# Optimization experiments

Hardware: AMD Instinct MI355X
Metric: run time of the kernel (lower is better)

The kernel has to match this reference:

```python
import jax, jax.numpy as jnp
import numpy as np

E, C_IN, NUM_CLASSES = 4, 3, 100
HW = 32
C1, C2, GC = 64, 128, 16
FC_IN = C2 * (HW // 4) * (HW // 4)  # 128*8*8 = 8192


def _conv(x, w, b):
    # x: [B,Cin,H,W], w: [Cout,Cin,3,3] -> [B,Cout,H,W] (SAME padding)
    y = jax.lax.conv_general_dilated(x, w, (1, 1), 'SAME',
                                     dimension_numbers=('NCHW', 'OIHW', 'NCHW'))
    return y + b[None, :, None, None]


def _maxpool2(x):
    return jax.lax.reduce_window(x, -jnp.inf, jax.lax.max,
                                 (1, 1, 2, 2), (1, 1, 2, 2), 'VALID')


def setup_inputs() -> dict:
    key = jax.random.key(0)
    ks = jax.random.split(key, 12)
    s = lambda k, shape, fan: (jax.random.normal(k, shape, jnp.float32) / np.sqrt(fan))
    return {
        'x': jax.random.normal(ks[0], (1024, C_IN, HW, HW), jnp.float32),
        # gating network
        'gate_cw': s(ks[1], (GC, C_IN, 3, 3), C_IN * 9),
        'gate_cb': jnp.zeros((GC,), jnp.float32),
        'gate_fw': s(ks[2], (E, GC), GC),
        'gate_fb': jnp.zeros((E,), jnp.float32),
        # stacked expert params [E, ...]
        'e_c1w': s(ks[3], (E, C1, C_IN, 3, 3), C_IN * 9),
        'e_c1b': jnp.zeros((E, C1), jnp.float32),
        'e_c2w': s(ks[4], (E, C2, C1, 3, 3), C1 * 9),
        'e_c2b': jnp.zeros((E, C2), jnp.float32),
        'e_fw': s(ks[5], (E, NUM_CLASSES, FC_IN), FC_IN),
        'e_fb': jnp.zeros((E, NUM_CLASSES), jnp.float32),
    }


def reference(x, gate_cw, gate_cb, gate_fw, gate_fb,
              e_c1w, e_c1b, e_c2w, e_c2b, e_fw, e_fb):
    B = x.shape[0]
    # --- gating: conv -> relu -> global avg pool -> linear -> softmax ---
    g = jax.nn.relu(_conv(x, gate_cw, gate_cb))            # [B,GC,H,W]
    g = g.mean(axis=(2, 3))                                # [B,GC]
    router_probs = jax.nn.softmax(g @ gate_fw.T + gate_fb) # [B,E]

    best_weights = router_probs.max(axis=1)                # [B]
    best_indices = jnp.argmax(router_probs, axis=1)        # [B]

    # --- hard top-1 dispatch: mask-and-combine (same math as gather/scatter) ---
    final_output = jnp.zeros((B, NUM_CLASSES), x.dtype)
    for e in range(E):  # fixed small expert count, structurally distinct params
        h = jax.nn.relu(_conv(x, e_c1w[e], e_c1b[e]))      # [B,64,32,32]
        h = _maxpool2(h)                                   # [B,64,16,16]
        h = jax.nn.relu(_conv(h, e_c2w[e], e_c2b[e]))      # [B,128,16,16]
        h = _maxpool2(h)                                   # [B,128,8,8]
        logits = h.reshape(B, -1) @ e_fw[e].T + e_fb[e]    # [B,100]
        mask = (best_indices == e)[:, None]
        final_output = final_output + jnp.where(
            mask, logits * best_weights[:, None], 0.0)

    mean_probs = router_probs.mean(axis=0)
    aux_loss = jnp.mean((mean_probs - 1.0 / E) ** 2)
    return final_output, router_probs, aux_loss
```

## Files before the change

kernel.cpp:

```cpp
#include <hip/hip_runtime.h>
#include <hip/hip_bf16.h>
#include <cstdint>


#define B_TOT 1024

typedef __attribute__((ext_vector_type(8))) short short8;
typedef __attribute__((ext_vector_type(16))) float f32x16;

__device__ __forceinline__ ushort f2bf(float f) {
  uint32_t u = __float_as_uint(f);
  u += 0x7fffu + ((u >> 16) & 1u);
  return (ushort)(u >> 16);
}

__global__ __launch_bounds__(256) void k_wprep(const float* __restrict__ w2,
                                               ushort* __restrict__ wp) {
  const int i = blockIdx.x * 256 + threadIdx.x;
  const int j = i & 7;
  const int cout = (i >> 3) & 127;
  const int kb = (i >> 10) & 7;
  const int kkE = i >> 13;
  const int kk = kkE - (kkE / 9) * 9;
  const int e = kkE / 9;
  const int ci = kb * 8 + j;
  const float f = w2[(size_t)(((e * 128 + cout) * 64 + ci) * 9) + kk];
  wp[i] = f2bf(f);
}

__global__ __launch_bounds__(256) void k_w1prep(const float* __restrict__ w1,
                                                ushort* __restrict__ wA) {
  const int i = blockIdx.x * 256 + threadIdx.x;
  const int j = i & 7;
  const int cout = (i >> 3) & 63;
  const int kb = (i >> 9) & 3;
  const int e = i >> 11;
  const int k = kb * 8 + j;
  float f = 0.f;
  if (k < 27) {
    const int ci = k / 9;
    const int kk = k - ci * 9;
    f = w1[(size_t)(((e * 64 + cout) * 3 + ci) * 9) + kk];
  }
  wA[i] = f2bf(f);
}

__global__ __launch_bounds__(256) void k_wfc(const float* __restrict__ efw,
                                             ushort* __restrict__ wfc) {
  const int i = blockIdx.x * 256 + threadIdx.x;
  const int j = i & 7;
  const int cout = (i >> 3) & 127;
  const int kb = (i >> 10) & 1023;
  const int e = i >> 20;
  const int k = kb * 8 + j;
  float f = 0.f;
  if (cout < 100) f = efw[((size_t)(e * 100 + cout)) * 8192 + k];
  wfc[i] = f2bf(f);
}

__global__ __launch_bounds__(256, 2) void k_gate(
    const float* __restrict__ x, const float* __restrict__ gcw,
    const float* __restrict__ gcb, float* __restrict__ g_mean) {
  __shared__ float xs[3 * 34 * 34];
  __shared__ float red[4 * 16];
  const int b = blockIdx.x;
  const int t = threadIdx.x;
  const float* xb = x + (size_t)b * 3072;

  for (int c = t; c < 3468; c += 256) {
    const int ci = c / 1156;
    const int rem = c - ci * 1156;
    const int y = rem / 34;
    const int xx = rem - y * 34;
    const int gy = y - 1, gx = xx - 1;
    float v = 0.f;
    if (gy >= 0 && gy < 32 && gx >= 0 && gx < 32) v = xb[ci * 1024 + gy * 32 + gx];
    xs[c] = v;
  }
  __syncthreads();

  const int r = t >> 3;
  const int c0 = (t & 7) * 4;

  float accp[16][4];
#pragma unroll
  for (int c = 0; c < 16; c++)
#pragma unroll
    for (int p = 0; p < 4; p++) accp[c][p] = 0.f;

#pragma unroll
  for (int ci = 0; ci < 3; ci++) {
    float pv[3][6];
#pragma unroll
    for (int dy = 0; dy < 3; dy++) {
      const float* row = xs + ci * 1156 + (r + dy) * 34 + c0;
#pragma unroll
      for (int dx = 0; dx < 6; dx++) pv[dy][dx] = row[dx];
    }
#pragma unroll
    for (int c = 0; c < 16; c++) {
      const float* wr = gcw + (c * 3 + ci) * 9;
#pragma unroll
      for (int ky = 0; ky < 3; ky++)
#pragma unroll
        for (int kx = 0; kx < 3; kx++) {
          const float wv = wr[ky * 3 + kx];
#pragma unroll
          for (int p = 0; p < 4; p++)
            accp[c][p] += wv * pv[ky][kx + p];
        }
    }
  }

  float sums[16];
#pragma unroll
  for (int c = 0; c < 16; c++) {
    const float bb = gcb[c];
    float s = 0.f;
#pragma unroll
    for (int p = 0; p < 4; p++) s += fmaxf(accp[c][p] + bb, 0.f);
    sums[c] = s;
  }

  const int wave = t >> 6, lane = t & 63;
#pragma unroll
  for (int c = 0; c < 16; c++) {
    float v = sums[c];
    for (int o = 32; o > 0; o >>= 1) v += __shfl_down(v, o);
    if (lane == 0) red[wave * 16 + c] = v;
  }
  __syncthreads();
  if (t < 16) {
    g_mean[b * 16 + t] =
        (red[t] + red[16 + t] + red[32 + t] + red[48 + t]) * (1.f / 1024.f);
  }
}

__global__ __launch_bounds__(256) void k_route(
    const float* __restrict__ g_mean, const float* __restrict__ gfw,
    const float* __restrict__ gfb, float* __restrict__ probs,
    float* __restrict__ best_w, int* __restrict__ best_idx,
    int* __restrict__ off_g, int* __restrict__ counts_g,
    int* __restrict__ order, float* __restrict__ aux_out) {
  __shared__ int cnt[4], ofs[5], cl[4];
  __shared__ short bidx[1024];
  __shared__ float red[16];
  const int t = threadIdx.x;
  if (t < 4) { cnt[t] = 0; cl[t] = 0; }
  __syncthreads();

  float asum[4] = {0.f, 0.f, 0.f, 0.f};
  for (int s = t; s < B_TOT; s += 256) {
    float g[16];
#pragma unroll
    for (int c = 0; c < 16; c++) g[c] = g_mean[s * 16 + c];
    float lg[4];
#pragma unroll
    for (int e = 0; e < 4; e++) {
      float sum = gfb[e];
#pragma unroll
      for (int c = 0; c < 16; c++) sum += g[c] * gfw[e * 16 + c];
      lg[e] = sum;
    }
    const float m = fmaxf(fmaxf(lg[0], lg[1]), fmaxf(lg[2], lg[3]));
    float ex[4], ssum = 0.f;
#pragma unroll
    for (int e = 0; e < 4; e++) { ex[e] = expf(lg[e] - m); ssum += ex[e]; }
    const float inv = 1.f / ssum;
    float p[4];
#pragma unroll
    for (int e = 0; e < 4; e++) {
      p[e] = ex[e] * inv;
      probs[s * 4 + e] = p[e];
      asum[e] += p[e];
    }
    int bi = 0; float bp = p[0];
#pragma unroll
    for (int e = 1; e < 4; e++) if (p[e] > bp) { bp = p[e]; bi = e; }
    best_w[s] = bp;
    best_idx[s] = bi;
    bidx[s] = (short)bi;
    atomicAdd(&cnt[bi], 1);
  }
  __syncthreads();

  if (t == 0) {
    int o = 0;
#pragma unroll
    for (int e = 0; e < 4; e++) { ofs[e] = o; o += ((cnt[e] + 31) & ~31); }
    ofs[4] = o;
#pragma unroll
    for (int i = 0; i < 5; i++) off_g[i] = ofs[i];
#pragma unroll
    for (int e = 0; e < 4; e++) counts_g[e] = cnt[e];
  }
  __syncthreads();

  for (int s = t; s < B_TOT; s += 256) {
    const int e2 = bidx[s];
    const int slot = ofs[e2] + atomicAdd(&cl[e2], 1);
    order[slot] = s;
  }

  const int wave = t >> 6, lane = t & 63;
#pragma unroll
  for (int e = 0; e < 4; e++) {
    float v = asum[e];
    for (int o = 32; o > 0; o >>= 1) v += __shfl_down(v, o);
    if (lane == 0) red[wave * 4 + e] = v;
  }
  __syncthreads();
  if (t == 0) {
    float aux = 0.f;
#pragma unroll
    for (int e = 0; e < 4; e++) {
      const float mp = (red[e] + red[4 + e] + red[8 + e] + red[12 + e]) * (1.f / 1024.f);
      const float d = mp - 0.25f;
      aux += d * d;
    }
    aux_out[0] = aux * 0.25f;
  }
}

__global__ __launch_bounds__(256) void k_conv1(
    const float* __restrict__ x, const ushort* __restrict__ wA,
    const float* __restrict__ b1, const int* __restrict__ best_idx,
    ushort* __restrict__ h1q) {
  __shared__ ushort xs[1020];
  __shared__ __align__(16) ushort Bl[256 * 32];
  const int blk = blockIdx.x;
  const int b = blk >> 2;
  const int q = blk & 3;
  const int t = threadIdx.x;
  const int e = __builtin_amdgcn_readfirstlane(best_idx[b]);
  const float* xb = x + (size_t)b * 3072;
  const float* b1e = b1 + (size_t)e * 64;

  for (int c = t; c < 1020; c += 256) {
    const int ci = c / 340;
    const int rem = c - ci * 340;
    const int hr = rem / 34;
    const int hc = rem - hr * 34;
    const int gr = 8 * q + hr - 1, gc = hc - 1;
    float v = 0.f;
    if (gr >= 0 && gr < 32 && gc >= 0 && gc < 32) v = xb[ci * 1024 + gr * 32 + gc];
    xs[c] = f2bf(v);
  }
  __syncthreads();

  {
    const int rr = t >> 5, cc = t & 31;
    ushort us[32];
#pragma unroll
    for (int k = 0; k < 32; k++) {
      ushort v = 0;
      if (k < 27) {
        const int ci = k / 9;
        const int tap = k - ci * 9;
        const int dy = tap / 3, dx = tap - dy * 3;
        v = xs[ci * 340 + (rr + dy) * 34 + cc + dx];
      }
      us[k] = v;
    }
    uint4 pk[2];
    uint* pu = (uint*)pk;
#pragma unroll
    for (int w = 0; w < 8; w++)
      pu[w] = (uint)us[w * 2] | ((uint)us[w * 2 + 1] << 16);
    *(uint4*)(Bl + t * 32) = pk[0];
    *(uint4*)(Bl + t * 32 + 8) = pk[1];
    uint4 pk2[2];
    uint* pu2 = (uint*)pk2;
#pragma unroll
    for (int w = 0; w < 8; w++)
      pu2[w] = (uint)us[16 + w * 2] | ((uint)us[16 + w * 2 + 1] << 16);
    *(uint4*)(Bl + t * 32 + 16) = pk2[0];
    *(uint4*)(Bl + t * 32 + 24) = pk2[1];
  }
  __syncthreads();

  const int lane = t & 63;
  const int wv = t >> 6;
  const int g = wv & 1;
  const int nh = wv >> 1;
  const int ln = lane & 31;
  const int half = lane >> 5;

  const short8 af0 = *(const short8*)(wA + (size_t)(((e * 4 + half) * 64) + g * 32 + ln) * 8);
  const short8 af1 = *(const short8*)(wA + (size_t)(((e * 4 + 2 + half) * 64) + g * 32 + ln) * 8);

  f32x16 acc[4];
#pragma unroll
  for (int tt = 0; tt < 4; tt++)
#pragma unroll
    for (int i = 0; i < 16; i++) acc[tt][i] = 0.f;

#pragma unroll
  for (int tt = 0; tt < 4; tt++) {
    const ushort* bcol = Bl + (size_t)((nh * 4 + tt) * 32 + ln) * 32;
    const short8 b0 = *(const short8*)(bcol + half * 8);
    const short8 b1v = *(const short8*)(bcol + 16 + half * 8);
    acc[tt] = __builtin_amdgcn_mfma_f32_32x32x16_bf16(af0, b0, acc[tt], 0, 0, 0);
    acc[tt] = __builtin_amdgcn_mfma_f32_32x32x16_bf16(af1, b1v, acc[tt], 0, 0, 0);
  }

  float bias[16];
#pragma unroll
  for (int r = 0; r < 16; r++)
    bias[r] = b1e[g * 32 + (r & 3) + 8 * (r >> 2) + 4 * half];

  const int pc = ln >> 1;
#pragma unroll
  for (int j = 0; j < 2; j++) {
    float pw[16];
#pragma unroll
    for (int r = 0; r < 16; r++) {
      float v = fmaxf(acc[2 * j][r], acc[2 * j + 1][r]);
      v = fmaxf(v, __shfl_xor(v, 1));
      pw[r] = fmaxf(v + bias[r], 0.f);
    }
    if ((lane & 1) == 0) {
      const int pos = (4 * q + nh * 2 + j) * 16 + pc;
      ushort* dst = h1q + (size_t)b * 16384 + pos * 8 + 4 * half;
#pragma unroll
      for (int rg = 0; rg < 4; rg++) {
        uint2 pk;
        pk.x = (uint)f2bf(pw[rg * 4 + 0]) | ((uint)f2bf(pw[rg * 4 + 1]) << 16);
        pk.y = (uint)f2bf(pw[rg * 4 + 2]) | ((uint)f2bf(pw[rg * 4 + 3]) << 16);
        *(uint2*)(dst + (g * 4 + rg) * 2048) = pk;
      }
    }
  }
}

__global__ __launch_bounds__(256, 2) void k_conv2(
    const ushort* __restrict__ h1q, const ushort* __restrict__ wp,
    const float* __restrict__ b2, const int* __restrict__ best_idx,
    ushort* __restrict__ h2q) {
  __shared__ uint4 st[1440];
  const int blk = blockIdx.x;
  const int b = blk >> 1;
  const int q = blk & 1;
  const int t = threadIdx.x;
  const int e = __builtin_amdgcn_readfirstlane(best_idx[b]);
  const ushort* wpe = wp + (size_t)e * 73728;

  for (int c = t; c < 1440; c += 256) {
    const int row = c / 144;
    const int rem = c - row * 144;
    const int cig = rem / 18;
    const int col = rem - cig * 18;
    const int gy = 8 * q - 1 + row, gx = col - 1;
    uint4 v = make_uint4(0u, 0u, 0u, 0u);
    if (gy >= 0 && gy < 16 && gx >= 0 && gx < 16)
      v = *(const uint4*)(h1q + (size_t)b * 16384 + cig * 2048 + (gy * 16 + gx) * 8);
    st[c] = v;
  }
  __syncthreads();

  const int lane = t & 63;
  const int wv = t >> 6;
  const int g = wv & 1;
  const int h = wv >> 1;
  const int half = lane >> 5;
  const int n = lane & 31;
  const int drow = n >> 4;
  const int col15 = n & 15;
  const int cm0 = g * 64;

  f32x16 acc[2][2];
#pragma unroll
  for (int m = 0; m < 2; m++)
#pragma unroll
    for (int nt = 0; nt < 2; nt++)
#pragma unroll
      for (int i = 0; i < 16; i++) acc[m][nt][i] = 0.f;

  const short* sbs = (const short*)st;
  const ushort* abase = wpe + (size_t)(half * 128 + cm0 + n) * 8;

  short8 a0[4], a1[4];
#pragma unroll
  for (int c4 = 0; c4 < 4; c4++) {
    a0[c4] = *(const short8*)(abase + c4 * 2048);
    a1[c4] = *(const short8*)(abase + c4 * 2048 + 256);
  }

#pragma unroll
  for (int kk = 0; kk < 9; kk++) {
    const int ky = kk / 3;
    const int kx = kk - ky * 3;
#pragma unroll
    for (int c4 = 0; c4 < 4; c4++) {
      const int kb = c4 * 2 + half;
#pragma unroll
      for (int nt = 0; nt < 2; nt++) {
        const int rin = 4 * h + 2 * nt + drow + ky;
        const int cin = col15 + kx;
        const short8 bf = *(const short8*)(sbs + ((rin * 8 + kb) * 18 + cin) * 8);
        acc[0][nt] = __builtin_amdgcn_mfma_f32_32x32x16_bf16(a0[c4], bf, acc[0][nt], 0, 0, 0);
        acc[1][nt] = __builtin_amdgcn_mfma_f32_32x32x16_bf16(a1[c4], bf, acc[1][nt], 0, 0, 0);
      }
      if (kk < 8) {
        a0[c4] = *(const short8*)(abase + (kk + 1) * 8192 + c4 * 2048);
        a1[c4] = *(const short8*)(abase + (kk + 1) * 8192 + c4 * 2048 + 256);
      }
    }
  }
  __syncthreads();

  ushort* pls = (ushort*)st;
#pragma unroll
  for (int m = 0; m < 2; m++)
#pragma unroll
    for (int nt = 0; nt < 2; nt++) {
#pragma unroll
      for (int r = 0; r < 16; r++) {
        float v = acc[m][nt][r];
        v = fmaxf(v, __shfl_xor(v, 1));
        v = fmaxf(v, __shfl_xor(v, 16));
        if ((lane & 17) == 0) {
          const int rowm = (r & 3) + 8 * (r >> 2) + 4 * half;
          const int cout = cm0 + m * 32 + rowm;
          const int prl = 2 * h + nt;
          const int pc = (n >> 1) & 7;
          pls[cout * 32 + prl * 8 + pc] = f2bf(fmaxf(v + b2[e * 128 + cout], 0.f));
        }
      }
    }
  __syncthreads();

  {
#pragma unroll
    for (int p = 0; p < 2; p++) {
      const int f16 = p * 256 + t;
      const int flat = f16 * 8;
      const int cout = flat >> 5;
      const int pos32 = flat & 31;
      uint4* dst = (uint4*)(h2q + (size_t)b * 8192 + cout * 64 + 32 * q + pos32);
      *dst = ((const uint4*)pls)[f16];
    }
  }
}

__global__ __launch_bounds__(256) void k_fc(
    const ushort* __restrict__ h2q, const ushort* __restrict__ wfc,
    const int* __restrict__ order, const int* __restrict__ off,
    const int* __restrict__ counts, float* __restrict__ partial) {
  __shared__ ushort bs[32 * 32 * 8];
  __shared__ int sid[32];
  const int tix = blockIdx.x;
  const int ks = blockIdx.y;
  const int base = tix * 32;
  if (base >= off[4]) return;
  int e = 0;
#pragma unroll
  for (int i = 1; i < 4; i++) if (base >= off[i]) e = i;
  const int vend = off[e] + counts[e];
  const int t = threadIdx.x;
  if (t < 32) {
    const int pos = base + t;
    sid[t] = (pos < vend) ? order[pos] : -1;
  }
  __syncthreads();

  const int lane = t & 63;
  const int wv = t >> 6;
  const int half = lane >> 5;
  const int mn = lane & 31;
  const int cout0 = wv * 32;
  const int ss = t & 31;
  const int kgrp = t >> 5;
  const int srow = sid[ss] >= 0 ? sid[ss] : 0;
  const ushort* arow = h2q + (size_t)srow * 8192;

  f32x16 acc;
#pragma unroll
  for (int i = 0; i < 16; i++) acc[i] = 0.f;

  const ushort* wbase = wfc + ((size_t)e * 1024 + (size_t)ks * 64) * 1024;
  const short* sb = (const short*)bs;

#pragma unroll
  for (int ch = 0; ch < 2; ch++) {
    const int k0g = ks * 512 + ch * 256;
    if (ch) __syncthreads();
#pragma unroll
    for (int p = 0; p < 4; p++) {
      const int kb = p * 8 + kgrp;
      const uint4 v = *(const uint4*)(arow + k0g + kb * 8);
      *(uint4*)(bs + (kb * 32 + ss) * 8) = v;
    }
    __syncthreads();
#pragma unroll
    for (int kk = 0; kk < 16; kk++) {
      const int kbl = kk * 2 + half;
      const short8 af = *(const short8*)(wbase +
          ((size_t)(ch * 32 + kbl) * 128 + cout0 + mn) * 8);
      const short8 bf = *(const short8*)(sb + (kbl * 32 + mn) * 8);
      acc = __builtin_amdgcn_mfma_f32_32x32x16_bf16(af, bf, acc, 0, 0, 0);
    }
  }

  float* pks = partial + (size_t)ks * 147456;
#pragma unroll
  for (int r = 0; r < 16; r++) {
    const int cout = cout0 + (r & 3) + 8 * (r >> 2) + 4 * half;
    pks[(size_t)cout * 1152 + base + mn] = acc[r];
  }
}

__global__ __launch_bounds__(256) void k_red(
    const float* __restrict__ partial, const float* __restrict__ efb,
    const int* __restrict__ order, const int* __restrict__ off,
    const int* __restrict__ counts, const float* __restrict__ best_w,
    float* __restrict__ out) {
  const int slot = blockIdx.x * 256 + threadIdx.x;
  if (slot >= off[4]) return;
  int e = 0;
#pragma unroll
  for (int i = 1; i < 4; i++) if (slot >= off[i]) e = i;
  if (slot - off[e] >= counts[e]) return;
  const int s = order[slot];
  const float bw = best_w[s];
  const int o0 = blockIdx.y * 4;
#pragma unroll
  for (int j = 0; j < 4; j++) {
    const int o = o0 + j;
    float sum = 0.f;
#pragma unroll
    for (int ks = 0; ks < 16; ks++)
      sum += partial[(size_t)ks * 147456 + (size_t)o * 1152 + slot];
    out[(size_t)s * 100 + o] = (sum + efb[e * 100 + o]) * bw;
  }
}

extern "C" void kernel_launch(void* const* d_in, const int* in_sizes, int n_in,
                              void* d_out, int out_size, void* d_ws, size_t ws_size,
                              hipStream_t stream) {
  const float* x   = (const float*)d_in[0];
  const float* gcw = (const float*)d_in[1];
  const float* gcb = (const float*)d_in[2];
  const float* gfw = (const float*)d_in[3];
  const float* gfb = (const float*)d_in[4];
  const float* c1w = (const float*)d_in[5];
  const float* c1b = (const float*)d_in[6];
  const float* c2w = (const float*)d_in[7];
  const float* c2b = (const float*)d_in[8];
  const float* efw = (const float*)d_in[9];
  const float* efb = (const float*)d_in[10];
  float* out = (float*)d_out;
  float* ws  = (float*)d_ws;

  float*  g_mean   = ws;
  float*  best_w   = ws + 16384;
  int*    best_idx = (int*)(ws + 17408);
  int*    counts   = (int*)(ws + 18432);
  int*    off      = (int*)(ws + 18440);
  int*    order    = (int*)(ws + 18448);
  ushort* wp       = (ushort*)(ws + 20480);
  ushort* wfc      = (ushort*)(ws + 167936);
  ushort* h1       = (ushort*)(ws + 2265088);
  ushort* h2q      = (ushort*)(ws + 10653696);
  float*  partial  = ws + 14848000;
  ushort* wA       = (ushort*)(ws + 17207296);

  float* probs = out + 102400;
  float* aux   = out + 106496;

  k_wprep<<<1152, 256, 0, stream>>>(c2w, wp);
  k_w1prep<<<128, 256, 0, stream>>>(c1w, wA);
  k_wfc<<<16384, 256, 0, stream>>>(efw, wfc);
  k_gate<<<1024, 256, 0, stream>>>(x, gcw, gcb, g_mean);
  k_route<<<1, 256, 0, stream>>>(g_mean, gfw, gfb, probs, best_w, best_idx,
                                 off, counts, order, aux);
  k_conv1<<<4096, 256, 0, stream>>>(x, wA, c1b, best_idx, h1);
  k_conv2<<<2048, 256, 0, stream>>>(h1, wp, c2b, best_idx, h2q);
  dim3 g5(36, 16);
  k_fc<<<g5, 256, 0, stream>>>(h2q, wfc, order, off, counts, partial);
  dim3 g6(5, 25);
  k_red<<<g6, 256, 0, stream>>>(partial, efb, order, off, counts, best_w, out);
}
```

Measured before the change: 229.7 us.

## Fuse conv1 and conv2 into one per-image kernel keeping h1 in LDS

Merges the conv1+pool and conv2+pool kernels into a single kernel with one block per image. The pooled conv1 output is written straight into a zero-padded shared-memory tile that conv2 reads, so the h1 intermediate never goes to global memory and back. Each block now computes the full 16x16 conv2 output with more accumulators per wave, which raises register and LDS pressure and leaves only 1024 blocks. Conv1 is processed in four row strips with extra barriers between them.

```diff
diff --git a/kernel.cpp b/kernel.cpp
--- a/kernel.cpp
+++ b/kernel.cpp
@@ -222,162 +222,141 @@
   }
 }
 
-__global__ __launch_bounds__(256) void k_conv1(
+__global__ __launch_bounds__(256, 2) void k_conv12(
     const float* __restrict__ x, const ushort* __restrict__ wA,
-    const float* __restrict__ b1, const int* __restrict__ best_idx,
-    ushort* __restrict__ h1q) {
-  __shared__ ushort xs[1020];
+    const float* __restrict__ b1, const ushort* __restrict__ wp,
+    const float* __restrict__ b2, const int* __restrict__ best_idx,
+    ushort* __restrict__ h2q) {
+  __shared__ ushort xs[3 * 34 * 34];
   __shared__ __align__(16) ushort Bl[256 * 32];
-  const int blk = blockIdx.x;
-  const int b = blk >> 2;
-  const int q = blk & 3;
+  __shared__ uint4 st[18 * 8 * 18];
+  const int b = blockIdx.x;
   const int t = threadIdx.x;
   const int e = __builtin_amdgcn_readfirstlane(best_idx[b]);
   const float* xb = x + (size_t)b * 3072;
-  const float* b1e = b1 + (size_t)e * 64;
-
-  for (int c = t; c < 1020; c += 256) {
-    const int ci = c / 340;
-    const int rem = c - ci * 340;
-    const int hr = rem / 34;
-    const int hc = rem - hr * 34;
-    const int gr = 8 * q + hr - 1, gc = hc - 1;
+
+  {
+    const uint4 z = make_uint4(0u, 0u, 0u, 0u);
+    for (int c = t; c < 2592; c += 256) st[c] = z;
+  }
+  for (int c = t; c < 3468; c += 256) {
+    const int ci = c / 1156;
+    const int rem = c - ci * 1156;
+    const int y = rem / 34;
+    const int xx = rem - y * 34;
+    const int gy = y - 1, gx = xx - 1;
     float v = 0.f;
-    if (gr >= 0 && gr < 32 && gc >= 0 && gc < 32) v = xb[ci * 1024 + gr * 32 + gc];
+    if (gy >= 0 && gy < 32 && gx >= 0 && gx < 32) v = xb[ci * 1024 + gy * 32 + gx];
     xs[c] = f2bf(v);
   }
-  __syncthreads();
-
-  {
-    const int rr = t >> 5, cc = t & 31;
-    ushort us[32];
-#pragma unroll
-    for (int k = 0; k < 32; k++) {
-      ushort v = 0;
-      if (k < 27) {
-        const int ci = k / 9;
-        const int tap = k - ci * 9;
-        const int dy = tap / 3, dx = tap - dy * 3;
-        v = xs[ci * 340 + (rr + dy) * 34 + cc + dx];
-      }
-      us[k] = v;
-    }
-    uint4 pk[2];
-    uint* pu = (uint*)pk;
-#pragma unroll
-    for (int w = 0; w < 8; w++)
-      pu[w] = (uint)us[w * 2] | ((uint)us[w * 2 + 1] << 16);
-    *(uint4*)(Bl + t * 32) = pk[0];
-    *(uint4*)(Bl + t * 32 + 8) = pk[1];
-    uint4 pk2[2];
-    uint* pu2 = (uint*)pk2;
-#pragma unroll
-    for (int w = 0; w < 8; w++)
-      pu2[w] = (uint)us[16 + w * 2] | ((uint)us[16 + w * 2 + 1] << 16);
-    *(uint4*)(Bl + t * 32 + 16) = pk2[0];
-    *(uint4*)(Bl + t * 32 + 24) = pk2[1];
-  }
-  __syncthreads();
 
   const int lane = t & 63;
   const int wv = t >> 6;
   const int g = wv & 1;
-  const int nh = wv >> 1;
   const int ln = lane & 31;
   const int half = lane >> 5;
 
   const short8 af0 = *(const short8*)(wA + (size_t)(((e * 4 + half) * 64) + g * 32 + ln) * 8);
   const short8 af1 = *(const short8*)(wA + (size_t)(((e * 4 + 2 + half) * 64) + g * 32 + ln) * 8);
-
-  f32x16 acc[4];
-#pragma unroll
-  for (int tt = 0; tt < 4; tt++)
-#pragma unroll
-    for (int i = 0; i < 16; i++) acc[tt][i] = 0.f;
-
-#pragma unroll
-  for (int tt = 0; tt < 4; tt++) {
-    const ushort* bcol = Bl + (size_t)((nh * 4 + tt) * 32 + ln) * 32;
-    const short8 b0 = *(const short8*)(bcol + half * 8);
-    const short8 b1v = *(const short8*)(bcol + 16 + half * 8);
-    acc[tt] = __builtin_amdgcn_mfma_f32_32x32x16_bf16(af0, b0, acc[tt], 0, 0, 0);
-    acc[tt] = __builtin_amdgcn_mfma_f32_32x32x16_bf16(af1, b1v, acc[tt], 0, 0, 0);
-  }
-
-  float bias[16];
+  const float* b1e = b1 + (size_t)e * 64;
+  float bias1[16];
 #pragma unroll
   for (int r = 0; r < 16; r++)
-    bias[r] = b1e[g * 32 + (r & 3) + 8 * (r >> 2) + 4 * half];
-
-  const int pc = ln >> 1;
-#pragma unroll
-  for (int j = 0; j < 2; j++) {
-    float pw[16];
-#pragma unroll
-    for (int r = 0; r < 16; r++) {
-      float v = fmaxf(acc[2 * j][r], acc[2 * j + 1][r]);
-      v = fmaxf(v, __shfl_xor(v, 1));
-      pw[r] = fmaxf(v + bias[r], 0.f);
-    }
-    if ((lane & 1) == 0) {
-      const int pos = (4 * q + nh * 2 + j) * 16 + pc;
-      ushort* dst = h1q + (size_t)b * 16384 + pos * 8 + 4 * half;
-#pragma unroll
-      for (int rg = 0; rg < 4; rg++) {
-        uint2 pk;
-        pk.x = (uint)f2bf(pw[rg * 4 + 0]) | ((uint)f2bf(pw[rg * 4 + 1]) << 16);
-        pk.y = (uint)f2bf(pw[rg * 4 + 2]) | ((uint)f2bf(pw[rg * 4 + 3]) << 16);
-        *(uint2*)(dst + (g * 4 + rg) * 2048) = pk;
+    bias1[r] = b1e[g * 32 + (r & 3) + 8 * (r >> 2) + 4 * half];
+
+  const int nh = wv >> 1;
+  const int rr = t >> 5, cc = t & 31;
+  ushort* stw = (ushort*)st;
+
+  for (int s = 0; s < 4; s++) {
+    __syncthreads();
+    {
+      ushort us[32];
+#pragma unroll
+      for (int k = 0; k < 32; k++) {
+        ushort v = 0;
+        if (k < 27) {
+          const int ci = k / 9;
+          const int tap = k - ci * 9;
+          const int dy = tap / 3, dx = tap - dy * 3;
+          v = xs[ci * 1156 + (8 * s + rr + dy) * 34 + cc + dx];
+        }
+        us[k] = v;
       }
-    }
-  }
-}
-
-__global__ __launch_bounds__(256, 2) void k_conv2(
-    const ushort* __restrict__ h1q, const ushort* __restrict__ wp,
-    const float* __restrict__ b2, const int* __restrict__ best_idx,
-    ushort* __restrict__ h2q) {
-  __shared__ uint4 st[1440];
-  const int blk = blockIdx.x;
-  const int b = blk >> 1;
-  const int q = blk & 1;
-  const int t = threadIdx.x;
-  const int e = __builtin_amdgcn_readfirstlane(best_idx[b]);
-  const ushort* wpe = wp + (size_t)e * 73728;
-
-  for (int c = t; c < 1440; c += 256) {
-    const int row = c / 144;
-    const int rem = c - row * 144;
-    const int cig = rem / 18;
-    const int col = rem - cig * 18;
-    const int gy = 8 * q - 1 + row, gx = col - 1;
-    uint4 v = make_uint4(0u, 0u, 0u, 0u);
-    if (gy >= 0 && gy < 16 && gx >= 0 && gx < 16)
-      v = *(const uint4*)(h1q + (size_t)b * 16384 + cig * 2048 + (gy * 16 + gx) * 8);
-    st[c] = v;
-  }
-  __syncthreads();
-
-  const int lane = t & 63;
-  const int wv = t >> 6;
-  const int g = wv & 1;
+      uint4 pk[2];
+      uint* pu = (uint*)pk;
+#pragma unroll
+      for (int w = 0; w < 8; w++)
+        pu[w] = (uint)us[w * 2] | ((uint)us[w * 2 + 1] << 16);
+      *(uint4*)(Bl + t * 32) = pk[0];
+      *(uint4*)(Bl + t * 32 + 8) = pk[1];
+      uint4 pk2[2];
+      uint* pu2 = (uint*)pk2;
+#pragma unroll
+      for (int w = 0; w < 8; w++)
+        pu2[w] = (uint)us[16 + w * 2] | ((uint)us[16 + w * 2 + 1] << 16);
+      *(uint4*)(Bl + t * 32 + 16) = pk2[0];
+      *(uint4*)(Bl + t * 32 + 24) = pk2[1];
+    }
+    __syncthreads();
+
+    f32x16 acc1[4];
+#pragma unroll
+    for (int tt = 0; tt < 4; tt++)
+#pragma unroll
+      for (int i = 0; i < 16; i++) acc1[tt][i] = 0.f;
+
+#pragma unroll
+    for (int tt = 0; tt < 4; tt++) {
+      const ushort* bcol = Bl + (size_t)((nh * 4 + tt) * 32 + ln) * 32;
+      const short8 b0 = *(const short8*)(bcol + half * 8);
+      const short8 b1v = *(const short8*)(bcol + 16 + half * 8);
+      acc1[tt] = __builtin_amdgcn_mfma_f32_32x32x16_bf16(af0, b0, acc1[tt], 0, 0, 0);
+      acc1[tt] = __builtin_amdgcn_mfma_f32_32x32x16_bf16(af1, b1v, acc1[tt], 0, 0, 0);
+    }
+
+    const int pc = ln >> 1;
+#pragma unroll
+    for (int j = 0; j < 2; j++) {
+      float pw[16];
+#pragma unroll
+      for (int r = 0; r < 16; r++) {
+        float v = fmaxf(acc1[2 * j][r], acc1[2 * j + 1][r]);
+        v = fmaxf(v, __shfl_xor(v, 1));
+        pw[r] = fmaxf(v + bias1[r], 0.f);
+      }
+      if ((lane & 1) == 0) {
+        const int prow = 4 * s + nh * 2 + j;
+#pragma unroll
+        for (int rg = 0; rg < 4; rg++) {
+          uint2 pk;
+          pk.x = (uint)f2bf(pw[rg * 4 + 0]) | ((uint)f2bf(pw[rg * 4 + 1]) << 16);
+          pk.y = (uint)f2bf(pw[rg * 4 + 2]) | ((uint)f2bf(pw[rg * 4 + 3]) << 16);
+          ushort* dst = stw +
+              ((size_t)((prow + 1) * 8 + (g * 4 + rg)) * 18 + (pc + 1)) * 8 + 4 * half;
+          *(uint2*)dst = pk;
+        }
+      }
+    }
+  }
+  __syncthreads();
+
   const int h = wv >> 1;
-  const int half = lane >> 5;
   const int n = lane & 31;
   const int drow = n >> 4;
   const int col15 = n & 15;
   const int cm0 = g * 64;
-
-  f32x16 acc[2][2];
-#pragma unroll
-  for (int m = 0; m < 2; m++)
-#pragma unroll
-    for (int nt = 0; nt < 2; nt++)
-#pragma unroll
-      for (int i = 0; i < 16; i++) acc[m][nt][i] = 0.f;
-
+  const ushort* wpe = wp + (size_t)e * 73728;
   const short* sbs = (const short*)st;
   const ushort* abase = wpe + (size_t)(half * 128 + cm0 + n) * 8;
+
+  f32x16 acc[2][4];
+#pragma unroll
+  for (int m = 0; m < 2; m++)
+#pragma unroll
+    for (int nt = 0; nt < 4; nt++)
+#pragma unroll
+      for (int i = 0; i < 16; i++) acc[m][nt][i] = 0.f;
 
   short8 a0[4], a1[4];
 #pragma unroll
@@ -394,8 +373,8 @@
     for (int c4 = 0; c4 < 4; c4++) {
       const int kb = c4 * 2 + half;
 #pragma unroll
-      for (int nt = 0; nt < 2; nt++) {
-        const int rin = 4 * h + 2 * nt + drow + ky;
+      for (int nt = 0; nt < 4; nt++) {
+        const int rin = 8 * h + 2 * nt + drow + ky;
         const int cin = col15 + kx;
         const short8 bf = *(const short8*)(sbs + ((rin * 8 + kb) * 18 + cin) * 8);
         acc[0][nt] = __builtin_amdgcn_mfma_f32_32x32x16_bf16(a0[c4], bf, acc[0][nt], 0, 0, 0);
@@ -407,13 +386,12 @@
       }
     }
   }
-  __syncthreads();
-
-  ushort* pls = (ushort*)st;
+
+  ushort* pls = (ushort*)Bl;
 #pragma unroll
   for (int m = 0; m < 2; m++)
 #pragma unroll
-    for (int nt = 0; nt < 2; nt++) {
+    for (int nt = 0; nt < 4; nt++) {
 #pragma unroll
       for (int r = 0; r < 16; r++) {
         float v = acc[m][nt][r];
@@ -422,24 +400,18 @@
         if ((lane & 17) == 0) {
           const int rowm = (r & 3) + 8 * (r >> 2) + 4 * half;
           const int cout = cm0 + m * 32 + rowm;
-          const int prl = 2 * h + nt;
-          const int pc = (n >> 1) & 7;
-          pls[cout * 32 + prl * 8 + pc] = f2bf(fmaxf(v + b2[e * 128 + cout], 0.f));
+          const int prl = 4 * h + nt;
+          const int pc2 = (n >> 1) & 7;
+          pls[cout * 64 + prl * 8 + pc2] = f2bf(fmaxf(v + b2[e * 128 + cout], 0.f));
         }
       }
     }
   __syncthreads();
 
-  {
-#pragma unroll
-    for (int p = 0; p < 2; p++) {
-      const int f16 = p * 256 + t;
-      const int flat = f16 * 8;
-      const int cout = flat >> 5;
-      const int pos32 = flat & 31;
-      uint4* dst = (uint4*)(h2q + (size_t)b * 8192 + cout * 64 + 32 * q + pos32);
-      *dst = ((const uint4*)pls)[f16];
-    }
+#pragma unroll
+  for (int p = 0; p < 4; p++) {
+    const int f16 = p * 256 + t;
+    *(uint4*)(h2q + (size_t)b * 8192 + f16 * 8) = ((const uint4*)pls)[f16];
   }
 }
 
@@ -560,7 +532,6 @@
   int*    order    = (int*)(ws + 18448);
   ushort* wp       = (ushort*)(ws + 20480);
   ushort* wfc      = (ushort*)(ws + 167936);
-  ushort* h1       = (ushort*)(ws + 2265088);
   ushort* h2q      = (ushort*)(ws + 10653696);
   float*  partial  = ws + 14848000;
   ushort* wA       = (ushort*)(ws + 17207296);
@@ -574,8 +545,7 @@
   k_gate<<<1024, 256, 0, stream>>>(x, gcw, gcb, g_mean);
   k_route<<<1, 256, 0, stream>>>(g_mean, gfw, gfb, probs, best_w, best_idx,
                                  off, counts, order, aux);
-  k_conv1<<<4096, 256, 0, stream>>>(x, wA, c1b, best_idx, h1);
-  k_conv2<<<2048, 256, 0, stream>>>(h1, wp, c2b, best_idx, h2q);
+  k_conv12<<<1024, 256, 0, stream>>>(x, wA, c1b, wp, c2b, best_idx, h2q);
   dim3 g5(36, 16);
   k_fc<<<g5, 256, 0, stream>>>(h2q, wfc, order, off, counts, partial);
   dim3 g6(5, 25);
```

Result: slower. 239.5 us (+4.3%).

## Split conv2 output channels into two passes to raise occupancy

Applied to the files above, without the earlier changes.

Conv2 now processes its 64 output channels per wave in two sequential 32-channel passes instead of one. This halves the live accumulator and A-fragment registers, which allows the launch bound to go from 2 to 4 blocks per CU. A separate shared buffer for the pooled output removes the barrier that reused the staging tile. In exchange, each B fragment is read from LDS twice and the weight loads run in two serialized chains, and the extra shared memory may itself limit occupancy.

```diff
diff --git a/kernel.cpp b/kernel.cpp
--- a/kernel.cpp
+++ b/kernel.cpp
@@ -333,11 +333,12 @@
   }
 }
 
-__global__ __launch_bounds__(256, 2) void k_conv2(
+__global__ __launch_bounds__(256, 4) void k_conv2(
     const ushort* __restrict__ h1q, const ushort* __restrict__ wp,
     const float* __restrict__ b2, const int* __restrict__ best_idx,
     ushort* __restrict__ h2q) {
   __shared__ uint4 st[1440];
+  __shared__ ushort pls[128 * 32];
   const int blk = blockIdx.x;
   const int b = blk >> 1;
   const int q = blk & 1;
@@ -368,66 +369,61 @@
   const int col15 = n & 15;
   const int cm0 = g * 64;
 
-  f32x16 acc[2][2];
-#pragma unroll
-  for (int m = 0; m < 2; m++)
-#pragma unroll
-    for (int nt = 0; nt < 2; nt++)
-#pragma unroll
-      for (int i = 0; i < 16; i++) acc[m][nt][i] = 0.f;
-
   const short* sbs = (const short*)st;
   const ushort* abase = wpe + (size_t)(half * 128 + cm0 + n) * 8;
 
-  short8 a0[4], a1[4];
-#pragma unroll
-  for (int c4 = 0; c4 < 4; c4++) {
-    a0[c4] = *(const short8*)(abase + c4 * 2048);
-    a1[c4] = *(const short8*)(abase + c4 * 2048 + 256);
-  }
-
-#pragma unroll
-  for (int kk = 0; kk < 9; kk++) {
-    const int ky = kk / 3;
-    const int kx = kk - ky * 3;
-#pragma unroll
-    for (int c4 = 0; c4 < 4; c4++) {
-      const int kb = c4 * 2 + half;
-#pragma unroll
-      for (int nt = 0; nt < 2; nt++) {
-        const int rin = 4 * h + 2 * nt + drow + ky;
-        const int cin = col15 + kx;
-        const short8 bf = *(const short8*)(sbs + ((rin * 8 + kb) * 18 + cin) * 8);
-        acc[0][nt] = __builtin_amdgcn_mfma_f32_32x32x16_bf16(a0[c4], bf, acc[0][nt], 0, 0, 0);
-        acc[1][nt] = __builtin_amdgcn_mfma_f32_32x32x16_bf16(a1[c4], bf, acc[1][nt], 0, 0, 0);
+#pragma unroll 1
+  for (int pm = 0; pm < 2; pm++) {
+    const ushort* am = abase + pm * 256;
+
+    f32x16 acc[2];
+#pragma unroll
+    for (int nt = 0; nt < 2; nt++)
+#pragma unroll
+      for (int i = 0; i < 16; i++) acc[nt][i] = 0.f;
+
+    short8 a[4];
+#pragma unroll
+    for (int c4 = 0; c4 < 4; c4++)
+      a[c4] = *(const short8*)(am + c4 * 2048);
+
+#pragma unroll
+    for (int kk = 0; kk < 9; kk++) {
+      const int ky = kk / 3;
+      const int kx = kk - ky * 3;
+#pragma unroll
+      for (int c4 = 0; c4 < 4; c4++) {
+        const int kb = c4 * 2 + half;
+#pragma unroll
+        for (int nt = 0; nt < 2; nt++) {
+          const int rin = 4 * h + 2 * nt + drow + ky;
+          const int cin = col15 + kx;
+          const short8 bf = *(const short8*)(sbs + ((rin * 8 + kb) * 18 + cin) * 8);
+          acc[nt] = __builtin_amdgcn_mfma_f32_32x32x16_bf16(a[c4], bf, acc[nt], 0, 0, 0);
+        }
+        if (kk < 8) {
+          a[c4] = *(const short8*)(am + (kk + 1) * 8192 + c4 * 2048);
+        }
       }
-      if (kk < 8) {
-        a0[c4] = *(const short8*)(abase + (kk + 1) * 8192 + c4 * 2048);
-        a1[c4] = *(const short8*)(abase + (kk + 1) * 8192 + c4 * 2048 + 256);
-      }
-    }
-  }
-  __syncthreads();
-
-  ushort* pls = (ushort*)st;
-#pragma unroll
-  for (int m = 0; m < 2; m++)
+    }
+
 #pragma unroll
     for (int nt = 0; nt < 2; nt++) {
 #pragma unroll
       for (int r = 0; r < 16; r++) {
-        float v = acc[m][nt][r];
+        float v = acc[nt][r];
         v = fmaxf(v, __shfl_xor(v, 1));
         v = fmaxf(v, __shfl_xor(v, 16));
         if ((lane & 17) == 0) {
           const int rowm = (r & 3) + 8 * (r >> 2) + 4 * half;
-          const int cout = cm0 + m * 32 + rowm;
+          const int cout = cm0 + pm * 32 + rowm;
           const int prl = 2 * h + nt;
           const int pc = (n >> 1) & 7;
           pls[cout * 32 + prl * 8 + pc] = f2bf(fmaxf(v + b2[e * 128 + cout], 0.f));
         }
       }
     }
+  }
   __syncthreads();
 
   {
```

Result: slower. 379.6 us (+65.3%).

## Fuse prep kernels into one launch and give conv2 one whole image per block

Applied to the files above, without the earlier changes.

The three weight-conversion kernels and the gating conv are merged into a single launch, with block ranges choosing which job each block does. This removes three kernel launches and the gaps between them. conv2 now uses one 512-thread block per image instead of two 256-thread blocks per half image, which removes the duplicated halo rows in the staging load and lets each block write contiguous output. The weight fragments are now streamed through a two-slot rolling prefetch instead of a four-slot one, so fewer registers hold weights, but loads are less far ahead and the larger blocks with more LDS may lower occupancy.

```diff
diff --git a/kernel.cpp b/kernel.cpp
--- a/kernel.cpp
+++ b/kernel.cpp
@@ -14,125 +14,123 @@
   return (ushort)(u >> 16);
 }
 
-__global__ __launch_bounds__(256) void k_wprep(const float* __restrict__ w2,
-                                               ushort* __restrict__ wp) {
-  const int i = blockIdx.x * 256 + threadIdx.x;
-  const int j = i & 7;
-  const int cout = (i >> 3) & 127;
-  const int kb = (i >> 10) & 7;
-  const int kkE = i >> 13;
-  const int kk = kkE - (kkE / 9) * 9;
-  const int e = kkE / 9;
-  const int ci = kb * 8 + j;
-  const float f = w2[(size_t)(((e * 128 + cout) * 64 + ci) * 9) + kk];
-  wp[i] = f2bf(f);
-}
-
-__global__ __launch_bounds__(256) void k_w1prep(const float* __restrict__ w1,
-                                                ushort* __restrict__ wA) {
-  const int i = blockIdx.x * 256 + threadIdx.x;
-  const int j = i & 7;
-  const int cout = (i >> 3) & 63;
-  const int kb = (i >> 9) & 3;
-  const int e = i >> 11;
-  const int k = kb * 8 + j;
-  float f = 0.f;
-  if (k < 27) {
-    const int ci = k / 9;
-    const int kk = k - ci * 9;
-    f = w1[(size_t)(((e * 64 + cout) * 3 + ci) * 9) + kk];
-  }
-  wA[i] = f2bf(f);
-}
-
-__global__ __launch_bounds__(256) void k_wfc(const float* __restrict__ efw,
-                                             ushort* __restrict__ wfc) {
-  const int i = blockIdx.x * 256 + threadIdx.x;
-  const int j = i & 7;
-  const int cout = (i >> 3) & 127;
-  const int kb = (i >> 10) & 1023;
-  const int e = i >> 20;
-  const int k = kb * 8 + j;
-  float f = 0.f;
-  if (cout < 100) f = efw[((size_t)(e * 100 + cout)) * 8192 + k];
-  wfc[i] = f2bf(f);
-}
-
-__global__ __launch_bounds__(256, 2) void k_gate(
+__global__ __launch_bounds__(256) void k_prep(
     const float* __restrict__ x, const float* __restrict__ gcw,
-    const float* __restrict__ gcb, float* __restrict__ g_mean) {
+    const float* __restrict__ gcb, float* __restrict__ g_mean,
+    const float* __restrict__ w2, ushort* __restrict__ wp,
+    const float* __restrict__ w1, ushort* __restrict__ wA,
+    const float* __restrict__ efw, ushort* __restrict__ wfc) {
   __shared__ float xs[3 * 34 * 34];
   __shared__ float red[4 * 16];
-  const int b = blockIdx.x;
+  const int blk = blockIdx.x;
   const int t = threadIdx.x;
-  const float* xb = x + (size_t)b * 3072;
-
-  for (int c = t; c < 3468; c += 256) {
-    const int ci = c / 1156;
-    const int rem = c - ci * 1156;
-    const int y = rem / 34;
-    const int xx = rem - y * 34;
-    const int gy = y - 1, gx = xx - 1;
-    float v = 0.f;
-    if (gy >= 0 && gy < 32 && gx >= 0 && gx < 32) v = xb[ci * 1024 + gy * 32 + gx];
-    xs[c] = v;
-  }
-  __syncthreads();
-
-  const int r = t >> 3;
-  const int c0 = (t & 7) * 4;
-
-  float accp[16][4];
-#pragma unroll
-  for (int c = 0; c < 16; c++)
-#pragma unroll
-    for (int p = 0; p < 4; p++) accp[c][p] = 0.f;
-
-#pragma unroll
-  for (int ci = 0; ci < 3; ci++) {
-    float pv[3][6];
-#pragma unroll
-    for (int dy = 0; dy < 3; dy++) {
-      const float* row = xs + ci * 1156 + (r + dy) * 34 + c0;
-#pragma unroll
-      for (int dx = 0; dx < 6; dx++) pv[dy][dx] = row[dx];
-    }
+
+  if (blk < 1024) {
+    const int b = blk;
+    const float* xb = x + (size_t)b * 3072;
+
+    for (int c = t; c < 3468; c += 256) {
+      const int ci = c / 1156;
+      const int rem = c - ci * 1156;
+      const int y = rem / 34;
+      const int xx = rem - y * 34;
+      const int gy = y - 1, gx = xx - 1;
+      float v = 0.f;
+      if (gy >= 0 && gy < 32 && gx >= 0 && gx < 32) v = xb[ci * 1024 + gy * 32 + gx];
+      xs[c] = v;
+    }
+    __syncthreads();
+
+    const int r = t >> 3;
+    const int c0 = (t & 7) * 4;
+
+    float accp[16][4];
+#pragma unroll
+    for (int c = 0; c < 16; c++)
+#pragma unroll
+      for (int p = 0; p < 4; p++) accp[c][p] = 0.f;
+
+#pragma unroll
+    for (int ci = 0; ci < 3; ci++) {
+      float pv[3][6];
+#pragma unroll
+      for (int dy = 0; dy < 3; dy++) {
+        const float* row = xs + ci * 1156 + (r + dy) * 34 + c0;
+#pragma unroll
+        for (int dx = 0; dx < 6; dx++) pv[dy][dx] = row[dx];
+      }
+#pragma unroll
+      for (int c = 0; c < 16; c++) {
+        const float* wr = gcw + (c * 3 + ci) * 9;
+#pragma unroll
+        for (int ky = 0; ky < 3; ky++)
+#pragma unroll
+          for (int kx = 0; kx < 3; kx++) {
+            const float wv = wr[ky * 3 + kx];
+#pragma unroll
+            for (int p = 0; p < 4; p++)
+              accp[c][p] += wv * pv[ky][kx + p];
+          }
+      }
+    }
+
+    float sums[16];
 #pragma unroll
     for (int c = 0; c < 16; c++) {
-      const float* wr = gcw + (c * 3 + ci) * 9;
-#pragma unroll
-      for (int ky = 0; ky < 3; ky++)
-#pragma unroll
-        for (int kx = 0; kx < 3; kx++) {
-          const float wv = wr[ky * 3 + kx];
-#pragma unroll
-          for (int p = 0; p < 4; p++)
-            accp[c][p] += wv * pv[ky][kx + p];
-        }
-    }
-  }
-
-  float sums[16];
-#pragma unroll
-  for (int c = 0; c < 16; c++) {
-    const float bb = gcb[c];
-    float s = 0.f;
-#pragma unroll
-    for (int p = 0; p < 4; p++) s += fmaxf(accp[c][p] + bb, 0.f);
-    sums[c] = s;
-  }
-
-  const int wave = t >> 6, lane = t & 63;
-#pragma unroll
-  for (int c = 0; c < 16; c++) {
-    float v = sums[c];
-    for (int o = 32; o > 0; o >>= 1) v += __shfl_down(v, o);
-    if (lane == 0) red[wave * 16 + c] = v;
-  }
-  __syncthreads();
-  if (t < 16) {
-    g_mean[b * 16 + t] =
-        (red[t] + red[16 + t] + red[32 + t] + red[48 + t]) * (1.f / 1024.f);
+      const float bb = gcb[c];
+      float s = 0.f;
+#pragma unroll
+      for (int p = 0; p < 4; p++) s += fmaxf(accp[c][p] + bb, 0.f);
+      sums[c] = s;
+    }
+
+    const int wave = t >> 6, lane = t & 63;
+#pragma unroll
+    for (int c = 0; c < 16; c++) {
+      float v = sums[c];
+      for (int o = 32; o > 0; o >>= 1) v += __shfl_down(v, o);
+      if (lane == 0) red[wave * 16 + c] = v;
+    }
+    __syncthreads();
+    if (t < 16) {
+      g_mean[b * 16 + t] =
+          (red[t] + red[16 + t] + red[32 + t] + red[48 + t]) * (1.f / 1024.f);
+    }
+  } else if (blk < 2176) {
+    const int i = (blk - 1024) * 256 + t;
+    const int j = i & 7;
+    const int cout = (i >> 3) & 127;
+    const int kb = (i >> 10) & 7;
+    const int kkE = i >> 13;
+    const int kk = kkE - (kkE / 9) * 9;
+    const int e = kkE / 9;
+    const int ci = kb * 8 + j;
+    const float f = w2[(size_t)(((e * 128 + cout) * 64 + ci) * 9) + kk];
+    wp[i] = f2bf(f);
+  } else if (blk < 2304) {
+    const int i = (blk - 2176) * 256 + t;
+    const int j = i & 7;
+    const int cout = (i >> 3) & 63;
+    const int kb = (i >> 9) & 3;
+    const int e = i >> 11;
+    const int k = kb * 8 + j;
+    float f = 0.f;
+    if (k < 27) {
+      const int ci = k / 9;
+      const int kk = k - ci * 9;
+      f = w1[(size_t)(((e * 64 + cout) * 3 + ci) * 9) + kk];
+    }
+    wA[i] = f2bf(f);
+  } else {
+    const int i = (blk - 2304) * 256 + t;
+    const int j = i & 7;
+    const int cout = (i >> 3) & 127;
+    const int kb = (i >> 10) & 1023;
+    const int e = i >> 20;
+    const int k = kb * 8 + j;
+    float f = 0.f;
+    if (cout < 100) f = efw[((size_t)(e * 100 + cout)) * 8192 + k];
+    wfc[i] = f2bf(f);
   }
 }
 
@@ -333,24 +331,22 @@
   }
 }
 
-__global__ __launch_bounds__(256, 2) void k_conv2(
+__global__ __launch_bounds__(512, 2) void k_conv2(
     const ushort* __restrict__ h1q, const ushort* __restrict__ wp,
     const float* __restrict__ b2, const int* __restrict__ best_idx,
     ushort* __restrict__ h2q) {
-  __shared__ uint4 st[1440];
-  const int blk = blockIdx.x;
-  const int b = blk >> 1;
-  const int q = blk & 1;
+  __shared__ uint4 st[2592];
+  const int b = blockIdx.x;
   const int t = threadIdx.x;
   const int e = __builtin_amdgcn_readfirstlane(best_idx[b]);
   const ushort* wpe = wp + (size_t)e * 73728;
 
-  for (int c = t; c < 1440; c += 256) {
+  for (int c = t; c < 2592; c += 512) {
     const int row = c / 144;
     const int rem = c - row * 144;
     const int cig = rem / 18;
     const int col = rem - cig * 18;
-    const int gy = 8 * q - 1 + row, gx = col - 1;
+    const int gy = row - 1, gx = col - 1;
     uint4 v = make_uint4(0u, 0u, 0u, 0u);
     if (gy >= 0 && gy < 16 && gx >= 0 && gx < 16)
       v = *(const uint4*)(h1q + (size_t)b * 16384 + cig * 2048 + (gy * 16 + gx) * 8);
@@ -368,43 +364,46 @@
   const int col15 = n & 15;
   const int cm0 = g * 64;
 
-  f32x16 acc[2][2];
-#pragma unroll
-  for (int m = 0; m < 2; m++)
-#pragma unroll
-    for (int nt = 0; nt < 2; nt++)
-#pragma unroll
-      for (int i = 0; i < 16; i++) acc[m][nt][i] = 0.f;
-
   const short* sbs = (const short*)st;
   const ushort* abase = wpe + (size_t)(half * 128 + cm0 + n) * 8;
 
-  short8 a0[4], a1[4];
-#pragma unroll
-  for (int c4 = 0; c4 < 4; c4++) {
-    a0[c4] = *(const short8*)(abase + c4 * 2048);
-    a1[c4] = *(const short8*)(abase + c4 * 2048 + 256);
-  }
-
-#pragma unroll
-  for (int kk = 0; kk < 9; kk++) {
+  f32x16 acc[2][2];
+#pragma unroll
+  for (int m = 0; m < 2; m++)
+#pragma unroll
+    for (int nt = 0; nt < 2; nt++)
+#pragma unroll
+      for (int i = 0; i < 16; i++) acc[m][nt][i] = 0.f;
+
+  short8 a0[2], a1[2];
+#pragma unroll
+  for (int s = 0; s < 2; s++) {
+    a0[s] = *(const short8*)(abase + s * 2048);
+    a1[s] = *(const short8*)(abase + s * 2048 + 256);
+  }
+
+#pragma unroll
+  for (int s = 0; s < 36; s++) {
+    const int kk = s >> 2;
+    const int c4 = s & 3;
     const int ky = kk / 3;
     const int kx = kk - ky * 3;
-#pragma unroll
-    for (int c4 = 0; c4 < 4; c4++) {
-      const int kb = c4 * 2 + half;
-#pragma unroll
-      for (int nt = 0; nt < 2; nt++) {
-        const int rin = 4 * h + 2 * nt + drow + ky;
-        const int cin = col15 + kx;
-        const short8 bf = *(const short8*)(sbs + ((rin * 8 + kb) * 18 + cin) * 8);
-        acc[0][nt] = __builtin_amdgcn_mfma_f32_32x32x16_bf16(a0[c4], bf, acc[0][nt], 0, 0, 0);
-        acc[1][nt] = __builtin_amdgcn_mfma_f32_32x32x16_bf16(a1[c4], bf, acc[1][nt], 0, 0, 0);
-      }
-      if (kk < 8) {
-        a0[c4] = *(const short8*)(abase + (kk + 1) * 8192 + c4 * 2048);
-        a1[c4] = *(const short8*)(abase + (kk + 1) * 8192 + c4 * 2048 + 256);
-      }
+    const int kb = c4 * 2 + half;
+    const int slot = s & 1;
+    const short8 ca0 = a0[slot];
+    const short8 ca1 = a1[slot];
+    if (s + 2 < 36) {
+      const int s2 = s + 2;
+      a0[slot] = *(const short8*)(abase + (s2 >> 2) * 8192 + (s2 & 3) * 2048);
+      a1[slot] = *(const short8*)(abase + (s2 >> 2) * 8192 + (s2 & 3) * 2048 + 256);
+    }
+#pragma unroll
+    for (int nt = 0; nt < 2; nt++) {
+      const int rin = 4 * h + 2 * nt + drow + ky;
+      const int cin = col15 + kx;
+      const short8 bf = *(const short8*)(sbs + ((rin * 8 + kb) * 18 + cin) * 8);
+      acc[0][nt] = __builtin_amdgcn_mfma_f32_32x32x16_bf16(ca0, bf, acc[0][nt], 0, 0, 0);
+      acc[1][nt] = __builtin_amdgcn_mfma_f32_32x32x16_bf16(ca1, bf, acc[1][nt], 0, 0, 0);
     }
   }
   __syncthreads();
@@ -424,22 +423,16 @@
           const int cout = cm0 + m * 32 + rowm;
           const int prl = 2 * h + nt;
           const int pc = (n >> 1) & 7;
-          pls[cout * 32 + prl * 8 + pc] = f2bf(fmaxf(v + b2[e * 128 + cout], 0.f));
+          pls[cout * 64 + prl * 8 + pc] = f2bf(fmaxf(v + b2[e * 128 + cout], 0.f));
         }
       }
     }
   __syncthreads();
 
-  {
-#pragma unroll
-    for (int p = 0; p < 2; p++) {
-      const int f16 = p * 256 + t;
-      const int flat = f16 * 8;
-      const int cout = flat >> 5;
-      const int pos32 = flat & 31;
-      uint4* dst = (uint4*)(h2q + (size_t)b * 8192 + cout * 64 + 32 * q + pos32);
-      *dst = ((const uint4*)pls)[f16];
-    }
+#pragma unroll
+  for (int p = 0; p < 2; p++) {
+    const int f16 = p * 512 + t;
+    *(uint4*)(h2q + (size_t)b * 8192 + f16 * 8) = ((const uint4*)pls)[f16];
   }
 }
 
@@ -568,14 +561,11 @@
   float* probs = out + 102400;
   float* aux   = out + 106496;
 
-  k_wprep<<<1152, 256, 0, stream>>>(c2w, wp);
-  k_w1prep<<<128, 256, 0, stream>>>(c1w, wA);
-  k_wfc<<<16384, 256, 0, stream>>>(efw, wfc);
-  k_gate<<<1024, 256, 0, stream>>>(x, gcw, gcb, g_mean);
+  k_prep<<<18688, 256, 0, stream>>>(x, gcw, gcb, g_mean, c2w, wp, c1w, wA, efw, wfc);
   k_route<<<1, 256, 0, stream>>>(g_mean, gfw, gfb, probs, best_w, best_idx,
                                  off, counts, order, aux);
   k_conv1<<<4096, 256, 0, stream>>>(x, wA, c1b, best_idx, h1);
-  k_conv2<<<2048, 256, 0, stream>>>(h1, wp, c2b, best_idx, h2q);
+  k_conv2<<<1024, 512, 0, stream>>>(h1, wp, c2b, best_idx, h2q);
   dim3 g5(36, 16);
   k_fc<<<g5, 256, 0, stream>>>(h2q, wfc, order, off, counts, partial);
   dim3 g6(5, 25);
```

Measured after the change: 228.4 us. No clear change (-0.6%).
